# Kernel tuning notes

Measured on AMD Instinct MI355X. Metric: run time of the kernel, lower is better.

Reference implementation:

```python
import jax, jax.numpy as jnp
import numpy as np

B, N = 2, 256
IN_N = 32          # input node features
H = 8              # per-layer default num_heads (GAT does not override it)
HN, HE = 64, 64    # hidden node / edge features per head
DN, DE = HN * H, HE * H  # 512, 512
OUT_N = 32


def _gat_layer(nodes, edges, mask, Wn, bn, We, be, Wa):
    # nodes: [b,n,dn_in], edges: [b,n,n,de_in], mask: [b,n] bool
    nf = nodes @ Wn + bn                                   # [b,n,DN]
    ef = jnp.einsum('bije,ef->bijf', edges, We) + be       # [b,n,n,DE]
    q = nf @ Wa                                            # [b,n,H]
    qe = jnp.einsum('bijf,fh->bijh', ef, Wa)               # [b,n,n,H]
    sn = jnp.einsum('bik,bjk->bij', q, q) / np.float32(np.sqrt(HN))
    se = jnp.einsum('bik,bijk->bij', q, qe) / np.float32(np.sqrt(HE))
    m = mask[..., None]
    wn = jax.nn.softmax(sn * m, axis=-1)                   # [b,n,n]
    we = jax.nn.softmax(se * m, axis=-1)                   # [b,n,n]
    awn = jnp.einsum('bij,bik->bjk', wn, nf)               # [b,n,DN]
    agg_e = jnp.einsum('bij,bijk->bik', we, ef)            # [b,n,DE]
    upd_nodes = nf + awn + agg_e                           # [b,n,DN]
    upd_edges = ef + we[..., None] * ef + jnp.einsum('bij,bik->bijk', wn, nf)
    re = jax.nn.elu(upd_edges)                             # [b,n,n,DE]
    re = (re + jnp.swapaxes(re, 1, 2)) / 2
    return jax.nn.elu(upd_nodes), re


def setup_inputs() -> dict:
    key = jax.random.key(0)
    ks = jax.random.split(key, 16)
    s = 0.05
    return {
        'nodes': jax.random.normal(ks[0], (B, N, IN_N), jnp.float32),
        'edges': jax.random.normal(ks[1], (B, N, N), jnp.float32),
        'node_mask': jnp.ones((B, N), dtype=bool),
        # layer 1 params
        'Wn1': jax.random.normal(ks[2], (IN_N, DN), jnp.float32) * s,
        'bn1': jnp.zeros((DN,), jnp.float32),
        'We1': jax.random.normal(ks[3], (1, DE), jnp.float32) * s,
        'be1': jnp.zeros((DE,), jnp.float32),
        'Wa1': jax.random.normal(ks[4], (DN, H), jnp.float32) * s,
        # layer 2 params
        'Wn2': jax.random.normal(ks[5], (DN, DN), jnp.float32) * s,
        'bn2': jnp.zeros((DN,), jnp.float32),
        'We2': jax.random.normal(ks[6], (DE, DE), jnp.float32) * s,
        'be2': jnp.zeros((DE,), jnp.float32),
        'Wa2': jax.random.normal(ks[7], (DN, H), jnp.float32) * s,
        # final projections
        'Wfn': jax.random.normal(ks[8], (DN, OUT_N), jnp.float32) * s,
        'bfn': jnp.zeros((OUT_N,), jnp.float32),
        'Wfe': jax.random.normal(ks[9], (DE, 1), jnp.float32) * s,
        'bfe': jnp.zeros((1,), jnp.float32),
    }


def reference(nodes, edges, node_mask, Wn1, bn1, We1, be1, Wa1,
              Wn2, bn2, We2, be2, Wa2, Wfn, bfn, Wfe, bfe):
    e = edges[..., None]                      # [b,n,n,1]
    e = (e + jnp.swapaxes(e, 1, 2)) / 2       # symmetrize
    e = jax.nn.relu(e)
    n, e = _gat_layer(nodes, e, node_mask, Wn1, bn1, We1, be1, Wa1)
    n, e = _gat_layer(n, e, node_mask, Wn2, bn2, We2, be2, Wa2)
    out_nodes = jnp.tanh(n @ Wfn + bfn)                                   # [b,n,OUT_N]
    out_edges = jnp.tanh(jnp.einsum('bijf,fo->bijo', e, Wfe) + bfe)[..., 0]  # [b,n,n]
    return out_nodes, out_edges
```

## Files before the change

kernel.cpp:

```cpp
#include <hip/hip_runtime.h>
#include <hip/hip_bf16.h>
#include <stdint.h>


typedef __attribute__((ext_vector_type(8))) short short8v;
typedef __attribute__((ext_vector_type(4))) float f32x4;

#define AS1 __attribute__((address_space(1)))
#define AS3 __attribute__((address_space(3)))

__device__ __forceinline__ float eluf(float x) { return x > 0.f ? x : (__expf(x) - 1.f); }

__device__ __forceinline__ short f2bf(float x) {
  union { float f; unsigned u; } v; v.f = x;
  unsigned r = v.u + 0x7fffu + ((v.u >> 16) & 1u);
  return (short)(r >> 16);
}

template<int OP>
__device__ float blockRed256(float v, float* s4) {
#pragma unroll
  for (int o = 32; o; o >>= 1) { float t = __shfl_xor(v, o); v = OP ? fmaxf(v, t) : v + t; }
  int w = threadIdx.x >> 6;
  __syncthreads();
  if ((threadIdx.x & 63) == 0) s4[w] = v;
  __syncthreads();
  return OP ? fmaxf(fmaxf(s4[0], s4[1]), fmaxf(s4[2], s4[3]))
            : (s4[0] + s4[1] + s4[2] + s4[3]);
}

__global__ __launch_bounds__(256) void k0m(const float* __restrict__ We2,
    const float* __restrict__ Wa2, const float* __restrict__ We1,
    const float* __restrict__ be1, const float* __restrict__ be2,
    const float* __restrict__ Wa1, short* __restrict__ Bp, float* __restrict__ M2,
    float* __restrict__ u1, float* __restrict__ v1, float* __restrict__ vb2) {
  int bid = blockIdx.x;
  if (bid < 128) {
    int id = bid * 256 + threadIdx.x;
    int c = id >> 11; int rem = id & 2047; int g = rem >> 9; int n = rem & 511;
    short8v v;
#pragma unroll
    for (int e = 0; e < 8; e++) v[e] = f2bf(We2[(c * 32 + g * 8 + e) * 512 + n]);
    int pos = n * 4 + (g ^ ((n >> 1) & 3));
    *(short8v*)(Bp + (c * 2048 + pos) * 8) = v;
    return;
  }
  int lane = threadIdx.x & 63;
  int idx = (bid - 128) * 4 + (threadIdx.x >> 6);
  if (idx < 512) {
    float a[8] = {0, 0, 0, 0, 0, 0, 0, 0};
    for (int k0 = lane; k0 < 512; k0 += 64) {
      float wv = We2[idx * 512 + k0];
      const float* wa = Wa2 + k0 * 8;
#pragma unroll
      for (int h = 0; h < 8; h++) a[h] += wv * wa[h];
    }
#pragma unroll
    for (int h = 0; h < 8; h++) {
      float v = a[h];
      for (int o = 32; o; o >>= 1) v += __shfl_xor(v, o);
      if (lane == 0) M2[idx * 8 + h] = v;
    }
  } else if (idx < 515) {
    const float* src = (idx == 512) ? We1 : (idx == 513 ? be1 : be2);
    const float* Wa = (idx == 514) ? Wa2 : Wa1;
    float* dst = (idx == 512) ? u1 : (idx == 513 ? v1 : vb2);
    float a[8] = {0, 0, 0, 0, 0, 0, 0, 0};
    for (int f = lane; f < 512; f += 64) {
      float s = src[f];
#pragma unroll
      for (int h = 0; h < 8; h++) a[h] += s * Wa[f * 8 + h];
    }
#pragma unroll
    for (int h = 0; h < 8; h++) {
      float v = a[h];
      for (int o = 32; o; o >>= 1) v += __shfl_xor(v, o);
      if (lane == 0) dst[h] = v;
    }
  }
}

__global__ __launch_bounds__(512) void k1_nf1(const float* __restrict__ nodes,
    const float* __restrict__ Wn1, const float* __restrict__ bn1,
    const float* __restrict__ Wa1, float* __restrict__ nf1, float* __restrict__ q1) {
  __shared__ float nrow[32];
  __shared__ float qL[8];
  int bi = blockIdx.x; int f = threadIdx.x;
  if (f < 32) nrow[f] = nodes[bi * 32 + f];
  if (f < 8) qL[f] = 0.f;
  __syncthreads();
  float acc = bn1[f];
#pragma unroll 8
  for (int c = 0; c < 32; c++) acc += nrow[c] * Wn1[c * 512 + f];
  nf1[bi * 512 + f] = acc;
  const float* wa = Wa1 + f * 8;
#pragma unroll
  for (int h = 0; h < 8; h++) {
    float v = acc * wa[h];
    for (int o = 32; o; o >>= 1) v += __shfl_xor(v, o);
    if ((f & 63) == 0) atomicAdd(&qL[h], v);
  }
  __syncthreads();
  if (f < 8) q1[bi * 8 + f] = qL[f];
}

__global__ __launch_bounds__(256) void k2_l1attn(const float* __restrict__ edges,
    const float* __restrict__ q1, const float* __restrict__ u1, const float* __restrict__ v1,
    float* __restrict__ e0, float* __restrict__ wn1, float* __restrict__ we1,
    float* __restrict__ tt) {
  __shared__ float s4[4];
  int bi = blockIdx.x; int b = bi >> 8; int i = bi & 255; int j = threadIdx.x;
  float qi[8], qj[8];
#pragma unroll
  for (int h = 0; h < 8; h++) { qi[h] = q1[bi * 8 + h]; qj[h] = q1[(b * 256 + j) * 8 + h]; }
  float eij = edges[bi * 256 + j];
  float eji = edges[(b * 256 + j) * 256 + i];
  float e0v = fmaxf(0.f, 0.5f * (eij + eji));
  e0[bi * 256 + j] = e0v;
  float sn = 0.f, aI = 0.f, cI = 0.f;
#pragma unroll
  for (int h = 0; h < 8; h++) { sn += qi[h] * qj[h]; aI += qi[h] * u1[h]; cI += qi[h] * v1[h]; }
  sn *= 0.125f;
  float se = (aI * e0v + cI) * 0.125f;
  float mn = blockRed256<1>(sn, s4);
  float en = __expf(sn - mn);
  float sumn = blockRed256<0>(en, s4);
  float wnv = en / sumn; wn1[bi * 256 + j] = wnv;
  float me = blockRed256<1>(se, s4);
  float ee = __expf(se - me);
  float sume = blockRed256<0>(ee, s4);
  float wev = ee / sume; we1[bi * 256 + j] = wev;
  float t = blockRed256<0>(wev * e0v, s4);
  if (j == 0) tt[bi] = t;
}

__global__ __launch_bounds__(512) void k34(const float* __restrict__ nf1,
    const float* __restrict__ wn1, const float* __restrict__ tt,
    const float* __restrict__ We1, const float* __restrict__ be1,
    const float* __restrict__ Wn2, const float* __restrict__ bn2,
    const float* __restrict__ Wa2, const float* __restrict__ M2,
    const float* __restrict__ vb2, float* __restrict__ nf2, float* __restrict__ q2,
    float* __restrict__ p2, float* __restrict__ cst) {
  __shared__ float n1L[2][512];
  __shared__ float qL[2][8];
  int bx = blockIdx.x;
  int b = bx >> 7; int x0 = (bx & 127) * 2; int k = threadIdx.x;
  int g0 = b * 256 + x0;
  float a0 = 0.f, a1 = 0.f;
#pragma unroll 4
  for (int i = 0; i < 256; i++) {
    float nv = nf1[(size_t)(b * 256 + i) * 512 + k];
    a0 += wn1[(b * 256 + i) * 256 + x0] * nv;
    a1 += wn1[(b * 256 + i) * 256 + x0 + 1] * nv;
  }
  float w = We1[k], be = be1[k];
  n1L[0][k] = eluf(nf1[(size_t)g0 * 512 + k] + a0 + tt[g0] * w + be);
  n1L[1][k] = eluf(nf1[(size_t)(g0 + 1) * 512 + k] + a1 + tt[g0 + 1] * w + be);
  if (k < 16) qL[k >> 3][k & 7] = 0.f;
  __syncthreads();
  float acc0 = bn2[k], acc1 = bn2[k];
#pragma unroll 4
  for (int g = 0; g < 512; g++) {
    float wv = Wn2[g * 512 + k];
    acc0 += n1L[0][g] * wv; acc1 += n1L[1][g] * wv;
  }
  nf2[(size_t)g0 * 512 + k] = acc0;
  nf2[(size_t)(g0 + 1) * 512 + k] = acc1;
  const float* wa = Wa2 + k * 8;
#pragma unroll
  for (int h = 0; h < 8; h++) {
    float v0 = acc0 * wa[h], v1 = acc1 * wa[h];
    for (int o = 32; o; o >>= 1) { v0 += __shfl_xor(v0, o); v1 += __shfl_xor(v1, o); }
    if ((k & 63) == 0) { atomicAdd(&qL[0][h], v0); atomicAdd(&qL[1][h], v1); }
  }
  __syncthreads();
  float q0[8], q1v[8];
#pragma unroll
  for (int h = 0; h < 8; h++) { q0[h] = qL[0][h]; q1v[h] = qL[1][h]; }
  if (k < 8) { q2[g0 * 8 + k] = q0[k]; q2[(g0 + 1) * 8 + k] = q1v[k]; }
  float p0 = 0.f, p1 = 0.f; const float* m2 = M2 + k * 8;
#pragma unroll
  for (int h = 0; h < 8; h++) { p0 += m2[h] * q0[h]; p1 += m2[h] * q1v[h]; }
  p2[(size_t)g0 * 512 + k] = p0;
  p2[(size_t)(g0 + 1) * 512 + k] = p1;
  if (k == 0) {
    float c0 = 0.f, c1 = 0.f;
#pragma unroll
    for (int h = 0; h < 8; h++) { c0 += q0[h] * vb2[h]; c1 += q1v[h] * vb2[h]; }
    cst[g0] = c0; cst[g0 + 1] = c1;
  }
}

__global__ __launch_bounds__(256) void k5b_pairs(const float* __restrict__ nf1,
    const float* __restrict__ p2, const float* __restrict__ e0,
    const float* __restrict__ wn1, const float* __restrict__ we1,
    const float* __restrict__ We1, const float* __restrict__ be1,
    const float* __restrict__ cst, float* __restrict__ se2) {
  __shared__ float NI[16 * 132], NJ[16 * 132], PI[16 * 132], PJ[16 * 132];
  __shared__ float W1[128], B1[128];
  int bid = blockIdx.x; int b = bid & 1; int pr = bid >> 1;
  int I = 0;
  { int p = pr; while (p >= 16 - I) { p -= 16 - I; I++; } pr = p; }
  int J = I + pr;
  int I0 = I * 16, J0 = J * 16;
  int tid = threadIdx.x; int ii = tid & 15, jj = tid >> 4;
  int gi = b * 256 + I0 + ii, gj = b * 256 + J0 + jj;
  int ij = gi * 256 + (J0 + jj), ji = gj * 256 + (I0 + ii);
  float e0v = e0[ij];
  float s1 = 1.f + we1[ij], w1 = wn1[ij];
  float s2 = 1.f + we1[ji], w2 = wn1[ji];
  float dot1 = 0.f, dot2 = 0.f;
  for (int fc = 0; fc < 4; fc++) {
    __syncthreads();
    int f00 = fc * 128;
    for (int t = tid; t < 2048; t += 256) {
      int row = t >> 7, f = t & 127;
      NI[row * 132 + f] = nf1[(size_t)(b * 256 + I0 + row) * 512 + f00 + f];
      NJ[row * 132 + f] = nf1[(size_t)(b * 256 + J0 + row) * 512 + f00 + f];
      PI[row * 132 + f] = p2[(size_t)(b * 256 + I0 + row) * 512 + f00 + f];
      PJ[row * 132 + f] = p2[(size_t)(b * 256 + J0 + row) * 512 + f00 + f];
    }
    if (tid < 128) { W1[tid] = We1[f00 + tid]; B1[tid] = be1[f00 + tid]; }
    __syncthreads();
#pragma unroll 8
    for (int f = 0; f < 128; f += 4) {
      float4 niv = *(const float4*)&NI[ii * 132 + f];
      float4 njv = *(const float4*)&NJ[jj * 132 + f];
      float4 piv = *(const float4*)&PI[ii * 132 + f];
      float4 pjv = *(const float4*)&PJ[jj * 132 + f];
      float4 wv = *(const float4*)&W1[f];
      float4 bv = *(const float4*)&B1[f];
      float ni_[4] = {niv.x, niv.y, niv.z, niv.w};
      float nj_[4] = {njv.x, njv.y, njv.z, njv.w};
      float pi_[4] = {piv.x, piv.y, piv.z, piv.w};
      float pj_[4] = {pjv.x, pjv.y, pjv.z, pjv.w};
      float w_[4] = {wv.x, wv.y, wv.z, wv.w};
      float b_[4] = {bv.x, bv.y, bv.z, bv.w};
#pragma unroll
      for (int e = 0; e < 4; e++) {
        float ef = e0v * w_[e] + b_[e];
        float x1 = ef * s1 + w1 * ni_[e];
        float x2 = ef * s2 + w2 * nj_[e];
        float e1v = 0.5f * (eluf(x1) + eluf(x2));
        dot1 += e1v * pi_[e];
        dot2 += e1v * pj_[e];
      }
    }
  }
  se2[ij] = (dot1 + cst[gi]) * 0.125f;
  se2[ji] = (dot2 + cst[gj]) * 0.125f;
}

__global__ __launch_bounds__(256) void k5ac(const float* __restrict__ q2,
    const float* __restrict__ se2, float* __restrict__ wn2, float* __restrict__ we2) {
  __shared__ float s4[4];
  int bi = blockIdx.x; int b = bi >> 8; int j = threadIdx.x;
  float sn = 0.f;
#pragma unroll
  for (int h = 0; h < 8; h++) sn += q2[bi * 8 + h] * q2[(b * 256 + j) * 8 + h];
  sn *= 0.125f;
  float mn = blockRed256<1>(sn, s4);
  float en = __expf(sn - mn);
  float s = blockRed256<0>(en, s4);
  wn2[bi * 256 + j] = en / s;
  float se = se2[bi * 256 + j];
  float me = blockRed256<1>(se, s4);
  float ee = __expf(se - me);
  float s2 = blockRed256<0>(ee, s4);
  we2[bi * 256 + j] = ee / s2;
}

__global__ __launch_bounds__(256) void kz(const float* __restrict__ nf1,
    const float* __restrict__ e0, const float* __restrict__ wn1,
    const float* __restrict__ we1, const float* __restrict__ we2,
    const float* __restrict__ We1, const float* __restrict__ be1, float* __restrict__ Z) {
  __shared__ float e0L[256], s1L[256], w1L[256], s2L[256], w2L[256], weL[256];
  int bi = blockIdx.x; int b = bi >> 8; int i = bi & 255; int tid = threadIdx.x;
  e0L[tid] = e0[bi * 256 + tid];
  s1L[tid] = 1.f + we1[bi * 256 + tid];
  w1L[tid] = wn1[bi * 256 + tid];
  weL[tid] = we2[bi * 256 + tid];
  s2L[tid] = 1.f + we1[(b * 256 + tid) * 256 + i];
  w2L[tid] = wn1[(b * 256 + tid) * 256 + i];
  __syncthreads();
  int k0 = tid, k1 = tid + 256;
  float W0 = We1[k0], B0 = be1[k0], W1 = We1[k1], B1 = be1[k1];
  float ni0 = nf1[(size_t)bi * 512 + k0], ni1 = nf1[(size_t)bi * 512 + k1];
  float z0 = 0.f, z1 = 0.f;
  const float* nfb = nf1 + (size_t)b * 256 * 512;
#pragma unroll 2
  for (int j = 0; j < 256; j++) {
    float e0v = e0L[j], s1 = s1L[j], w1 = w1L[j], s2 = s2L[j], w2 = w2L[j], we = weL[j];
    const float* nj = nfb + (size_t)j * 512;
    float nj0 = nj[k0], nj1 = nj[k1];
    float ef0 = e0v * W0 + B0;
    float x10 = ef0 * s1 + w1 * ni0, x20 = ef0 * s2 + w2 * nj0;
    z0 += we * 0.5f * (eluf(x10) + eluf(x20));
    float ef1 = e0v * W1 + B1;
    float x11 = ef1 * s1 + w1 * ni1, x21 = ef1 * s2 + w2 * nj1;
    z1 += we * 0.5f * (eluf(x11) + eluf(x21));
  }
  Z[(size_t)bi * 512 + k0] = z0;
  Z[(size_t)bi * 512 + k1] = z1;
}

__global__ __launch_bounds__(512, 2) void k6_main(
    const float* __restrict__ nf1, const float* __restrict__ nf2,
    const float* __restrict__ e0, const float* __restrict__ wn1, const float* __restrict__ we1,
    const float* __restrict__ wn2, const float* __restrict__ we2,
    const float* __restrict__ We1, const float* __restrict__ be1, const float* __restrict__ be2,
    const float* __restrict__ Wfe, const short* __restrict__ Bp,
    float* __restrict__ Dout) {
  __shared__ __align__(16) short As[2][4096];
  __shared__ __align__(16) short Bs[2][16384];
  __shared__ float We1L[512], be1L[512];
  __shared__ float e0r[128], s1r[128], w1r[128], s2r[128], w2r[128];
  __shared__ float weAr[128], wnAr[128], weBr[128], wnBr[128];
  __shared__ float dsumA[128], dsumB[128];

  int bid = blockIdx.x;
  int b = bid & 1; int rest = bid >> 1;
  int Jh = rest & 1; int pr = rest >> 1;
  int I = 0;
  { int p = pr; while (p >= 16 - I) { p -= 16 - I; I++; } pr = p; }
  int J = I + pr;
  int I0 = I * 16, J0 = J * 16 + Jh * 8;
  bool dual = (I != J);

  int tid = threadIdx.x, lane = tid & 63, w = tid >> 6;
  int wm = w >> 2, wn_ = w & 3;
  int g4 = lane >> 4;

  We1L[tid] = We1[tid]; be1L[tid] = be1[tid];
  if (tid < 128) {
    int i = I0 + (tid & 15), j = J0 + (tid >> 4);
    int ij = (b * 256 + i) * 256 + j, ji = (b * 256 + j) * 256 + i;
    e0r[tid] = e0[ij];
    s1r[tid] = 1.f + we1[ij]; w1r[tid] = wn1[ij];
    s2r[tid] = 1.f + we1[ji]; w2r[tid] = wn1[ji];
    weAr[tid] = we2[ij]; wnAr[tid] = wn2[ij];
    weBr[tid] = we2[ji]; wnBr[tid] = wn2[ji];
    dsumA[tid] = 0.f; dsumB[tid] = 0.f;
  }
  __syncthreads();

  int ar = tid >> 2;
  int ac = tid & 3;
  const float* nib = nf1 + (size_t)(b * 256 + I0 + (ar & 15)) * 512;
  const float* njb = nf1 + (size_t)(b * 256 + J0 + (ar >> 4)) * 512;
  float e0v = e0r[ar], s1 = s1r[ar], w1 = w1r[ar], s2 = s2r[ar], w2 = w2r[ar];
  int apos8 = (ar * 4 + (ac ^ ((ar >> 1) & 3))) * 8;

  auto genA = [&](int cg, short* dst) {
    int f0 = cg * 32 + ac * 8;
    float4 gi0 = *(const float4*)(nib + f0);
    float4 gi1 = *(const float4*)(nib + f0 + 4);
    float4 gj0 = *(const float4*)(njb + f0);
    float4 gj1 = *(const float4*)(njb + f0 + 4);
    float niv[8] = {gi0.x, gi0.y, gi0.z, gi0.w, gi1.x, gi1.y, gi1.z, gi1.w};
    float njv[8] = {gj0.x, gj0.y, gj0.z, gj0.w, gj1.x, gj1.y, gj1.z, gj1.w};
    float Wv[8], bv[8];
    *(float4*)&Wv[0] = *(const float4*)&We1L[f0];
    *(float4*)&Wv[4] = *(const float4*)&We1L[f0 + 4];
    *(float4*)&bv[0] = *(const float4*)&be1L[f0];
    *(float4*)&bv[4] = *(const float4*)&be1L[f0 + 4];
    short8v pk;
#pragma unroll
    for (int e = 0; e < 8; e++) {
      float ef = e0v * Wv[e] + bv[e];
      float x1 = ef * s1 + w1 * niv[e];
      float x2 = ef * s2 + w2 * njv[e];
      float v = 0.5f * (eluf(x1) + eluf(x2));
      pk[e] = f2bf(v);
    }
    *(short8v*)(dst + apos8) = pk;
  };
  auto stageB = [&](int cg, short* dstB) {
    const char* g = (const char*)(Bp + cg * 16384);
#pragma unroll
    for (int it = 0; it < 4; ++it) {
      int off = it * 8192 + w * 1024;
      __builtin_amdgcn_global_load_lds(
          (const AS1 void*)(g + off + lane * 16),
          (AS3 void*)((char*)dstB + off), 16, 0, 0);
    }
  };

  f32x4 acc[4][8];
#pragma unroll
  for (int mi = 0; mi < 4; mi++)
#pragma unroll
    for (int nf = 0; nf < 8; nf++) acc[mi][nf] = (f32x4){0.f, 0.f, 0.f, 0.f};

  genA(0, As[0]);
  stageB(0, Bs[0]);
  __syncthreads();

  for (int c = 0; c < 16; ++c) {
    int cur = c & 1, nxt = cur ^ 1;
    if (c < 15) {
      genA(c + 1, As[nxt]);
      stageB(c + 1, Bs[nxt]);
    }
    short8v a[4];
#pragma unroll
    for (int mi = 0; mi < 4; mi++) {
      int row = wm * 64 + mi * 16 + (lane & 15);
      int cpos = row * 4 + (g4 ^ ((row >> 1) & 3));
      a[mi] = *(const short8v*)(As[cur] + cpos * 8);
    }
#pragma unroll
    for (int nf = 0; nf < 8; nf++) {
      int n = wn_ * 128 + nf * 16 + (lane & 15);
      int pos = n * 4 + (g4 ^ ((n >> 1) & 3));
      short8v bf = *(const short8v*)(Bs[cur] + pos * 8);
#pragma unroll
      for (int mi = 0; mi < 4; mi++)
        acc[mi][nf] = __builtin_amdgcn_mfma_f32_16x16x32_bf16(a[mi], bf, acc[mi][nf], 0, 0, 0);
    }
    __syncthreads();
  }

  float be2v[8], wfev[8];
#pragma unroll
  for (int nf = 0; nf < 8; nf++) {
    int k = wn_ * 128 + nf * 16 + (lane & 15);
    be2v[nf] = be2[k]; wfev[nf] = Wfe[k];
  }
#pragma unroll
  for (int mi = 0; mi < 4; mi++) {
    int jRow = J0 + wm * 4 + mi;
    const float* nf2j = nf2 + (size_t)(b * 256 + jRow) * 512;
#pragma unroll
    for (int r4 = 0; r4 < 4; r4++) {
      int jl = wm * 64 + mi * 16 + g4 * 4 + r4;
      int iRow = I0 + g4 * 4 + r4;
      const float* nf2i = nf2 + (size_t)(b * 256 + iRow) * 512;
      float sEA = 1.f + weAr[jl], wNA = wnAr[jl];
      float sEB = 1.f + weBr[jl], wNB = wnBr[jl];
      float dvA = 0.f, dvB = 0.f;
#pragma unroll
      for (int nf = 0; nf < 8; nf++) {
        int k = wn_ * 128 + nf * 16 + (lane & 15);
        float ef2 = acc[mi][nf][r4] + be2v[nf];
        float UA = ef2 * sEA + wNA * nf2i[k];
        dvA += eluf(UA) * wfev[nf];
        if (dual) {
          float UB = ef2 * sEB + wNB * nf2j[k];
          dvB += eluf(UB) * wfev[nf];
        }
      }
#pragma unroll
      for (int o = 1; o < 16; o <<= 1) dvA += __shfl_xor(dvA, o);
      if ((lane & 15) == 0) atomicAdd(&dsumA[jl], dvA);
      if (dual) {
#pragma unroll
        for (int o = 1; o < 16; o <<= 1) dvB += __shfl_xor(dvB, o);
        if ((lane & 15) == 0) atomicAdd(&dsumB[jl], dvB);
      }
    }
  }
  __syncthreads();
  if (tid < 128) {
    int i = I0 + (tid & 15), j = J0 + (tid >> 4);
    Dout[(size_t)(b * 256 + i) * 256 + j] = dsumA[tid];
    if (dual) Dout[(size_t)(b * 256 + j) * 256 + i] = dsumB[tid];
  }
}

__global__ __launch_bounds__(512) void k78(const float* __restrict__ nf2,
    const float* __restrict__ wn2, const float* __restrict__ Z,
    const float* __restrict__ We2, const float* __restrict__ be2,
    const float* __restrict__ Wfn, const float* __restrict__ bfn,
    float* __restrict__ outn) {
  __shared__ float zL[2][512];
  __shared__ float n2L[2][512];
  __shared__ float red[512];
  int bx = blockIdx.x; int b = bx >> 7; int x0 = (bx & 127) * 2; int k = threadIdx.x;
  int g0 = b * 256 + x0;
  zL[0][k] = Z[(size_t)g0 * 512 + k];
  zL[1][k] = Z[(size_t)(g0 + 1) * 512 + k];
  float a0 = 0.f, a1 = 0.f;
#pragma unroll 4
  for (int i = 0; i < 256; i++) {
    float nv = nf2[(size_t)(b * 256 + i) * 512 + k];
    a0 += wn2[(b * 256 + i) * 256 + x0] * nv;
    a1 += wn2[(b * 256 + i) * 256 + x0 + 1] * nv;
  }
  __syncthreads();
  float ag0 = be2[k], ag1 = be2[k];
#pragma unroll 4
  for (int g = 0; g < 512; g++) {
    float wv = We2[g * 512 + k];
    ag0 += zL[0][g] * wv; ag1 += zL[1][g] * wv;
  }
  n2L[0][k] = eluf(nf2[(size_t)g0 * 512 + k] + a0 + ag0);
  n2L[1][k] = eluf(nf2[(size_t)(g0 + 1) * 512 + k] + a1 + ag1);
  __syncthreads();
  int row = k >> 8, t = k & 255;
  int o = t & 31, part = t >> 5;
  float acc = 0.f;
  for (int f = part * 64; f < part * 64 + 64; f++) acc += n2L[row][f] * Wfn[f * 32 + o];
  red[k] = acc;
  __syncthreads();
  if (k < 64) {
    int r2 = k >> 5, o2 = k & 31;
    float s = 0.f;
#pragma unroll
    for (int p = 0; p < 8; p++) s += red[r2 * 256 + p * 32 + o2];
    outn[(size_t)(g0 + r2) * 32 + o2] = tanhf(s + bfn[o2]);
  }
}

__global__ __launch_bounds__(256) void k9_oute(const float* __restrict__ D,
    const float* __restrict__ bfe, float* __restrict__ oute) {
  int bi = blockIdx.x; int b = bi >> 8; int i = bi & 255; int j = threadIdx.x;
  float v = 0.5f * (D[bi * 256 + j] + D[(b * 256 + j) * 256 + i]) + bfe[0];
  oute[bi * 256 + j] = tanhf(v);
}

extern "C" void kernel_launch(void* const* d_in, const int* in_sizes, int n_in,
                              void* d_out, int out_size, void* d_ws, size_t ws_size,
                              hipStream_t stream) {
  const float* nodes = (const float*)d_in[0];
  const float* edges = (const float*)d_in[1];
  const float* Wn1 = (const float*)d_in[3];
  const float* bn1 = (const float*)d_in[4];
  const float* We1 = (const float*)d_in[5];
  const float* be1 = (const float*)d_in[6];
  const float* Wa1 = (const float*)d_in[7];
  const float* Wn2 = (const float*)d_in[8];
  const float* bn2 = (const float*)d_in[9];
  const float* We2 = (const float*)d_in[10];
  const float* be2 = (const float*)d_in[11];
  const float* Wa2 = (const float*)d_in[12];
  const float* Wfn = (const float*)d_in[13];
  const float* bfn = (const float*)d_in[14];
  const float* Wfe = (const float*)d_in[15];
  const float* bfe = (const float*)d_in[16];

  float* ws = (float*)d_ws;
  size_t off = 0;
  float* nf1 = ws + off; off += 262144;
  float* q1 = ws + off; off += 4096;
  float* e0 = ws + off; off += 131072;
  float* wn1 = ws + off; off += 131072;
  float* we1 = ws + off; off += 131072;
  float* tt = ws + off; off += 512;
  float* nf2 = ws + off; off += 262144;
  float* q2 = ws + off; off += 4096;
  float* p2 = ws + off; off += 262144;
  float* cst = ws + off; off += 512;
  float* wn2 = ws + off; off += 131072;
  float* we2 = ws + off; off += 131072;
  float* M2 = ws + off; off += 4096;
  float* u1 = ws + off; off += 8;
  float* v1 = ws + off; off += 8;
  float* vb2 = ws + off; off += 16;
  float* se2 = ws + off; off += 131072;
  float* Zb = ws + off; off += 262144;
  float* Dm = ws + off; off += 131072;
  short* Bp = (short*)(ws + off); off += 131072;

  float* outn = (float*)d_out;
  float* oute = outn + 2 * 256 * 32;

  hipLaunchKernelGGL(k0m, dim3(257), dim3(256), 0, stream, We2, Wa2, We1, be1, be2, Wa1,
                     Bp, M2, u1, v1, vb2);
  hipLaunchKernelGGL(k1_nf1, dim3(512), dim3(512), 0, stream, nodes, Wn1, bn1, Wa1, nf1, q1);
  hipLaunchKernelGGL(k2_l1attn, dim3(512), dim3(256), 0, stream, edges, q1, u1, v1, e0, wn1,
                     we1, tt);
  hipLaunchKernelGGL(k34, dim3(256), dim3(512), 0, stream, nf1, wn1, tt, We1, be1,
                     Wn2, bn2, Wa2, M2, vb2, nf2, q2, p2, cst);
  hipLaunchKernelGGL(k5b_pairs, dim3(272), dim3(256), 0, stream, nf1, p2, e0, wn1, we1, We1,
                     be1, cst, se2);
  hipLaunchKernelGGL(k5ac, dim3(512), dim3(256), 0, stream, q2, se2, wn2, we2);
  hipLaunchKernelGGL(kz, dim3(512), dim3(256), 0, stream, nf1, e0, wn1, we1, we2, We1, be1,
                     Zb);
  hipLaunchKernelGGL(k6_main, dim3(544), dim3(512), 0, stream, nf1, nf2, e0, wn1, we1, wn2,
                     we2, We1, be1, be2, Wfe, Bp, Dm);
  hipLaunchKernelGGL(k78, dim3(256), dim3(512), 0, stream, nf2, wn2, Zb, We2, be2, Wfn, bfn,
                     outn);
  hipLaunchKernelGGL(k9_oute, dim3(512), dim3(256), 0, stream, Dm, bfe, oute);
}
```

Measured before the change: 358.5 us.

## Fuse edge output epilogue into k6 and stage node rows in LDS

k6_main now loads the 16 I-rows and 8 J-rows of nf1 into shared memory once and reads them from there when generating the A tiles, instead of reading global memory repeatedly. For off-diagonal tile pairs it computes the symmetrized tanh edge output directly and writes both (i,j) and (j,i). A small k9d kernel then handles only the diagonal tiles. This removes the full-size D round trip and most of the final edge kernel, but the roughly 50KB of added LDS per block may lower occupancy below the two blocks per CU the launch bounds target.

```diff
diff --git a/kernel.cpp b/kernel.cpp
--- a/kernel.cpp
+++ b/kernel.cpp
@@ -309,10 +309,12 @@
     const float* __restrict__ e0, const float* __restrict__ wn1, const float* __restrict__ we1,
     const float* __restrict__ wn2, const float* __restrict__ we2,
     const float* __restrict__ We1, const float* __restrict__ be1, const float* __restrict__ be2,
-    const float* __restrict__ Wfe, const short* __restrict__ Bp,
-    float* __restrict__ Dout) {
+    const float* __restrict__ Wfe, const float* __restrict__ bfe,
+    const short* __restrict__ Bp, float* __restrict__ Dout, float* __restrict__ oute) {
   __shared__ __align__(16) short As[2][4096];
   __shared__ __align__(16) short Bs[2][16384];
+  __shared__ float nfI[16][516];
+  __shared__ float nfJ[8][516];
   __shared__ float We1L[512], be1L[512];
   __shared__ float e0r[128], s1r[128], w1r[128], s2r[128], w2r[128];
   __shared__ float weAr[128], wnAr[128], weBr[128], wnBr[128];
@@ -332,6 +334,10 @@
   int g4 = lane >> 4;
 
   We1L[tid] = We1[tid]; be1L[tid] = be1[tid];
+  for (int t = tid; t < 16 * 512; t += 512)
+    nfI[t >> 9][t & 511] = nf1[(size_t)(b * 256 + I0 + (t >> 9)) * 512 + (t & 511)];
+  for (int t = tid; t < 8 * 512; t += 512)
+    nfJ[t >> 9][t & 511] = nf1[(size_t)(b * 256 + J0 + (t >> 9)) * 512 + (t & 511)];
   if (tid < 128) {
     int i = I0 + (tid & 15), j = J0 + (tid >> 4);
     int ij = (b * 256 + i) * 256 + j, ji = (b * 256 + j) * 256 + i;
@@ -346,17 +352,17 @@
 
   int ar = tid >> 2;
   int ac = tid & 3;
-  const float* nib = nf1 + (size_t)(b * 256 + I0 + (ar & 15)) * 512;
-  const float* njb = nf1 + (size_t)(b * 256 + J0 + (ar >> 4)) * 512;
+  const float* niL = &nfI[ar & 15][0];
+  const float* njL = &nfJ[ar >> 4][0];
   float e0v = e0r[ar], s1 = s1r[ar], w1 = w1r[ar], s2 = s2r[ar], w2 = w2r[ar];
   int apos8 = (ar * 4 + (ac ^ ((ar >> 1) & 3))) * 8;
 
   auto genA = [&](int cg, short* dst) {
     int f0 = cg * 32 + ac * 8;
-    float4 gi0 = *(const float4*)(nib + f0);
-    float4 gi1 = *(const float4*)(nib + f0 + 4);
-    float4 gj0 = *(const float4*)(njb + f0);
-    float4 gj1 = *(const float4*)(njb + f0 + 4);
+    float4 gi0 = *(const float4*)(niL + f0);
+    float4 gi1 = *(const float4*)(niL + f0 + 4);
+    float4 gj0 = *(const float4*)(njL + f0);
+    float4 gj1 = *(const float4*)(njL + f0 + 4);
     float niv[8] = {gi0.x, gi0.y, gi0.z, gi0.w, gi1.x, gi1.y, gi1.z, gi1.w};
     float njv[8] = {gj0.x, gj0.y, gj0.z, gj0.w, gj1.x, gj1.y, gj1.z, gj1.w};
     float Wv[8], bv[8];
@@ -463,9 +469,23 @@
   __syncthreads();
   if (tid < 128) {
     int i = I0 + (tid & 15), j = J0 + (tid >> 4);
-    Dout[(size_t)(b * 256 + i) * 256 + j] = dsumA[tid];
-    if (dual) Dout[(size_t)(b * 256 + j) * 256 + i] = dsumB[tid];
-  }
+    if (dual) {
+      float v = tanhf(0.5f * (dsumA[tid] + dsumB[tid]) + bfe[0]);
+      oute[(size_t)(b * 256 + i) * 256 + j] = v;
+      oute[(size_t)(b * 256 + j) * 256 + i] = v;
+    } else {
+      Dout[(size_t)(b * 256 + i) * 256 + j] = dsumA[tid];
+    }
+  }
+}
+
+__global__ __launch_bounds__(256) void k9d(const float* __restrict__ D,
+    const float* __restrict__ bfe, float* __restrict__ oute) {
+  int bid = blockIdx.x; int b = bid >> 4; int I0 = (bid & 15) * 16;
+  int r = threadIdx.x >> 4, c = threadIdx.x & 15;
+  int gi = b * 256 + I0 + r, gj = b * 256 + I0 + c;
+  float v = 0.5f * (D[(size_t)gi * 256 + I0 + c] + D[(size_t)gj * 256 + I0 + r]) + bfe[0];
+  oute[(size_t)gi * 256 + I0 + c] = tanhf(v);
 }
 
 __global__ __launch_bounds__(512) void k78(const float* __restrict__ nf2,
@@ -510,13 +530,6 @@
     for (int p = 0; p < 8; p++) s += red[r2 * 256 + p * 32 + o2];
     outn[(size_t)(g0 + r2) * 32 + o2] = tanhf(s + bfn[o2]);
   }
-}
-
-__global__ __launch_bounds__(256) void k9_oute(const float* __restrict__ D,
-    const float* __restrict__ bfe, float* __restrict__ oute) {
-  int bi = blockIdx.x; int b = bi >> 8; int i = bi & 255; int j = threadIdx.x;
-  float v = 0.5f * (D[bi * 256 + j] + D[(b * 256 + j) * 256 + i]) + bfe[0];
-  oute[bi * 256 + j] = tanhf(v);
 }
 
 extern "C" void kernel_launch(void* const* d_in, const int* in_sizes, int n_in,
@@ -578,8 +591,8 @@
   hipLaunchKernelGGL(kz, dim3(512), dim3(256), 0, stream, nf1, e0, wn1, we1, we2, We1, be1,
                      Zb);
   hipLaunchKernelGGL(k6_main, dim3(544), dim3(512), 0, stream, nf1, nf2, e0, wn1, we1, wn2,
-                     we2, We1, be1, be2, Wfe, Bp, Dm);
+                     we2, We1, be1, be2, Wfe, bfe, Bp, Dm, oute);
   hipLaunchKernelGGL(k78, dim3(256), dim3(512), 0, stream, nf2, wn2, Zb, We2, be2, Wfn, bfn,
                      outn);
-  hipLaunchKernelGGL(k9_oute, dim3(512), dim3(256), 0, stream, Dm, bfe, oute);
-}
+  hipLaunchKernelGGL(k9d, dim3(32), dim3(256), 0, stream, Dm, bfe, oute);
+}
```

Result: no change. 352.1 us (-1.8%).
